# Optimization experiments

Measured on AMD Instinct MI355X. Metric: run time of the kernel, lower is better.

The kernel has to match this reference:

```python
import jax, jax.numpy as jnp
import numpy as np

H = 32        # num_attention_heads (query heads)
G = 8         # num_query_groups (KV heads)
D = 128       # head_dim
HID = 4096    # hidden_size
THETA = 10000.0


def _rope(x, pos):
    # x: [B, h, S, D]; pos: [S]. Rotate-half (LLaMA) convention.
    half = D // 2
    inv_freq = 1.0 / (THETA ** (jnp.arange(0, half, dtype=jnp.float32) / half))
    ang = pos[:, None].astype(jnp.float32) * inv_freq[None, :]   # [S, half]
    cos = jnp.cos(ang)[None, None]                               # [1,1,S,half]
    sin = jnp.sin(ang)[None, None]
    x1, x2 = x[..., :half], x[..., half:]
    return jnp.concatenate([x1 * cos - x2 * sin, x1 * sin + x2 * cos], axis=-1)


def setup_inputs() -> dict:
    key = jax.random.key(0)
    ks = jax.random.split(key, 9)
    s = 0.02
    return {
        "hidden_states": jax.random.normal(ks[0], (1, 2048, HID), jnp.float32),
        "Wq": jax.random.normal(ks[1], (HID, H * D), jnp.float32) * s,
        "bq": jnp.zeros((H * D,), jnp.float32),
        "Wk": jax.random.normal(ks[2], (HID, G * D), jnp.float32) * s,
        "bk": jnp.zeros((G * D,), jnp.float32),
        "Wv": jax.random.normal(ks[3], (HID, G * D), jnp.float32) * s,
        "bv": jnp.zeros((G * D,), jnp.float32),
        "Wo": jax.random.normal(ks[4], (H * D, HID), jnp.float32) * s,
        "bo": jnp.zeros((HID,), jnp.float32),
    }


def reference(hidden_states, Wq, bq, Wk, bk, Wv, bv, Wo, bo):
    B, S, _ = hidden_states.shape
    R = H // G  # query heads per KV group

    q = hidden_states @ Wq + bq  # [B,S,H*D]
    k = hidden_states @ Wk + bk  # [B,S,G*D]
    v = hidden_states @ Wv + bv  # [B,S,G*D]

    q = q.reshape(B, S, H, D).transpose(0, 2, 1, 3)  # [B,H,S,D]
    k = k.reshape(B, S, G, D).transpose(0, 2, 1, 3)  # [B,G,S,D]
    v = v.reshape(B, S, G, D).transpose(0, 2, 1, 3)  # [B,G,S,D]

    pos = jnp.arange(S)
    q = _rope(q, pos)
    k = _rope(k, pos)

    # Grouped attention: broadcast KV across the R query heads of each group
    qg = q.reshape(B, G, R, S, D)
    scores = jnp.einsum('bgrsd,bgtd->bgrst', qg, k) / jnp.sqrt(jnp.float32(D))
    causal = jnp.tril(jnp.ones((S, S), dtype=bool))
    scores = jnp.where(causal[None, None, None], scores, jnp.finfo(scores.dtype).min)
    probs = jax.nn.softmax(scores, axis=-1)
    ctx = jnp.einsum('bgrst,bgtd->bgrsd', probs, v)          # [B,G,R,S,D]
    ctx = ctx.reshape(B, H, S, D).transpose(0, 2, 1, 3).reshape(B, S, H * D)
    return ctx @ Wo + bo
```

## Files before the change

### kernel.cpp

```cpp
#include <hip/hip_runtime.h>
#include <hip/hip_bf16.h>
#include <math.h>

#define HID   4096
#define NH    32
#define NG    8
#define DH    128
#define SEQ   2048
#define QKV_N 6144
#define KOFF  4096
#define VOFF  5120

typedef __bf16 bf16x8 __attribute__((ext_vector_type(8)));
typedef float  f32x4  __attribute__((ext_vector_type(4)));
using bf16 = __hip_bfloat16;

#define LOG2E 1.4426950408889634f
#define SCALE 0.08838834764831845f

typedef const __attribute__((address_space(1))) void* gas_p;
typedef __attribute__((address_space(3))) void* las_p;
__device__ __forceinline__ void async_copy16(void* lds, const void* g) {
  __builtin_amdgcn_global_load_lds((gas_p)g, (las_p)lds, 16, 0, 0);
}

__device__ __forceinline__ unsigned pack2(float a, float b) {
  union { bf16 h[2]; unsigned u; } t;
  t.h[0] = __float2bfloat16(a);
  t.h[1] = __float2bfloat16(b);
  return t.u;
}

__global__ void cast_x_kernel(const float* __restrict__ x, bf16* __restrict__ y, int n4) {
  int i = blockIdx.x * blockDim.x + threadIdx.x;
  if (i >= n4) return;
  float4 v = ((const float4*)x)[i];
  union { bf16 h[4]; uint2 u; } t;
  t.h[0] = __float2bfloat16(v.x);
  t.h[1] = __float2bfloat16(v.y);
  t.h[2] = __float2bfloat16(v.z);
  t.h[3] = __float2bfloat16(v.w);
  ((uint2*)y)[i] = t.u;
}

__global__ __launch_bounds__(256) void wtrans_all_kernel(const float* __restrict__ Wq, const float* __restrict__ Wk,
                                                         const float* __restrict__ Wv, const float* __restrict__ Wo,
                                                         bf16* __restrict__ Wqkv_t, bf16* __restrict__ Wot) {
  __shared__ bf16 T[64][72];
  const int bx = blockIdx.x;
  const float* W; bf16* dst; int N, ntile;
  if (bx < 64)      { W = Wq; dst = Wqkv_t;                      N = 4096; ntile = bx; }
  else if (bx < 80) { W = Wk; dst = Wqkv_t + (size_t)KOFF * HID; N = 1024; ntile = bx - 64; }
  else if (bx < 96) { W = Wv; dst = Wqkv_t + (size_t)VOFF * HID; N = 1024; ntile = bx - 80; }
  else              { W = Wo; dst = Wot;                         N = 4096; ntile = bx - 96; }
  const int n0 = ntile * 64, k0 = blockIdx.y * 64;
  const int t = threadIdx.x;
  const int nn = (t & 15) * 4, kk = t >> 4;
#pragma unroll
  for (int p = 0; p < 4; ++p) {
    const int k = kk + p * 16;
    float4 v = *(const float4*)&W[(size_t)(k0 + k) * N + n0 + nn];
    union { bf16 h[4]; uint2 u; } c;
    c.h[0] = __float2bfloat16(v.x);
    c.h[1] = __float2bfloat16(v.y);
    c.h[2] = __float2bfloat16(v.z);
    c.h[3] = __float2bfloat16(v.w);
    *(uint2*)&T[k][nn] = c.u;
  }
  __syncthreads();
  const int kc = t & 7, nr = t >> 3;
#pragma unroll
  for (int p = 0; p < 2; ++p) {
    const int n = nr + p * 32;
    union { bf16 h[8]; uint4 u; } o;
#pragma unroll
    for (int i = 0; i < 8; ++i) o.h[i] = T[kc * 8 + i][n];
    *(uint4*)&dst[(size_t)(n0 + n) * HID + k0 + kc * 8] = o.u;
  }
}

__global__ void bias_concat_kernel(const float* __restrict__ bq, const float* __restrict__ bk,
                                   const float* __restrict__ bv, float* __restrict__ dst) {
  int i = blockIdx.x * blockDim.x + threadIdx.x;
  if (i < 4096)       dst[i] = bq[i];
  else if (i < 5120)  dst[i] = bk[i - 4096];
  else if (i < 6144)  dst[i] = bv[i - 5120];
}

__device__ __forceinline__ void st_out(float* C, size_t idx, float v) { C[idx] = v; }
__device__ __forceinline__ void st_out(bf16*  C, size_t idx, float v) { C[idx] = __float2bfloat16(v); }

template <typename OutT>
__global__ __launch_bounds__(256) void gemm_bt_kernel(const bf16* __restrict__ A, const bf16* __restrict__ Bt,
                                                      const float* __restrict__ bias, OutT* __restrict__ C,
                                                      int M, int N, int K) {
  __shared__ alignas(16) bf16 As[128][32];
  __shared__ alignas(16) bf16 Bs[128][32];
  const int tid = threadIdx.x;
  const int w = tid >> 6, lane = tid & 63, quad = lane >> 4, l16 = lane & 15;
  const int wr = w >> 1, wc = w & 1;
  const int m0 = blockIdx.y * 128, n0 = blockIdx.x * 128;
  const int srow = lane >> 2;
  const int scol = (lane & 3) * 8;

  f32x4 acc[4][4];
  f32x4 zero4 = {0.f, 0.f, 0.f, 0.f};
#pragma unroll
  for (int mt = 0; mt < 4; ++mt)
#pragma unroll
    for (int nt = 0; nt < 4; ++nt) acc[mt][nt] = zero4;

  const int nIter = K >> 5;
  for (int kb = 0; kb < nIter; ++kb) {
    const int k0 = kb << 5;
#pragma unroll
    for (int c = 0; c < 2; ++c) {
      const int rb = w * 16 + c * 64;
      async_copy16(&As[rb][0], A  + (size_t)(m0 + rb + srow) * K + k0 + scol);
      async_copy16(&Bs[rb][0], Bt + (size_t)(n0 + rb + srow) * K + k0 + scol);
    }
    __syncthreads();
    bf16x8 af[4], bfr[4];
#pragma unroll
    for (int i = 0; i < 4; ++i) {
      af[i]  = *(const bf16x8*)&As[wr * 64 + i * 16 + l16][quad * 8];
      bfr[i] = *(const bf16x8*)&Bs[wc * 64 + i * 16 + l16][quad * 8];
    }
#pragma unroll
    for (int mt = 0; mt < 4; ++mt)
#pragma unroll
      for (int nt = 0; nt < 4; ++nt)
        acc[mt][nt] = __builtin_amdgcn_mfma_f32_16x16x32_bf16(af[mt], bfr[nt], acc[mt][nt], 0, 0, 0);
    __syncthreads();
  }

#pragma unroll
  for (int nt = 0; nt < 4; ++nt) {
    const int col = n0 + wc * 64 + nt * 16 + l16;
    const float bv = bias[col];
#pragma unroll
    for (int mt = 0; mt < 4; ++mt) {
#pragma unroll
      for (int r = 0; r < 4; ++r) {
        const int row = m0 + wr * 64 + mt * 16 + quad * 4 + r;
        st_out(C, (size_t)row * N + col, acc[mt][nt][r] + bv);
      }
    }
  }
}

__global__ __launch_bounds__(256) void rope_vtrans_kernel(bf16* __restrict__ qkv, bf16* __restrict__ vt) {
  __shared__ bf16 tle[32][33];
  const int bx = blockIdx.x;
  const int tid = threadIdx.x;
  if (bx < 2560) {
    int t = bx * 256 + tid;
    int c  = t & 7;
    int hs = (t >> 3) % 40;
    int s  = t / 320;
    int base = (hs < 32) ? hs * 128 : KOFF + (hs - 32) * 128;
    bf16* p = qkv + (size_t)s * QKV_N + base + c * 8;
    union { bf16x8 v; bf16 h[8]; } a, b, ra, rb;
    a.v = *(bf16x8*)p;
    b.v = *(bf16x8*)(p + 64);
#pragma unroll
    for (int j = 0; j < 8; ++j) {
      int d = c * 8 + j;
      float inv = expf(d * -0.14391156862f);
      float ang = (float)s * inv;
      float sn, cs;
      sincosf(ang, &sn, &cs);
      float x1 = __bfloat162float(a.h[j]);
      float x2 = __bfloat162float(b.h[j]);
      ra.h[j] = __float2bfloat16(x1 * cs - x2 * sn);
      rb.h[j] = __float2bfloat16(x1 * sn + x2 * cs);
    }
    *(bf16x8*)p        = ra.v;
    *(bf16x8*)(p + 64) = rb.v;
  } else {
    const int b = bx - 2560;
    const int s0 = (b & 63) * 32, d0 = ((b >> 6) & 3) * 32, g = b >> 8;
    const int tx = tid & 31, ty = tid >> 5;
#pragma unroll
    for (int i = 0; i < 4; ++i)
      tle[ty + i * 8][tx] = qkv[(size_t)(s0 + ty + i * 8) * QKV_N + VOFF + g * 128 + d0 + tx];
    __syncthreads();
#pragma unroll
    for (int i = 0; i < 4; ++i)
      vt[(size_t)(g * 128 + d0 + ty + i * 8) * SEQ + s0 + tx] = tle[tx][ty + i * 8];
  }
}

__global__ __launch_bounds__(256, 2) void attn_kernel(const bf16* __restrict__ qkv, const bf16* __restrict__ vt,
                                                      bf16* __restrict__ ctx) {
  __shared__ bf16 Ks[2][64][128];
  __shared__ bf16 Vs[2][128][64];

  const int bx = blockIdx.x;
  const int h  = blockIdx.y;
  const int g  = h >> 2;
  const int tid = threadIdx.x, w = tid >> 6, lane = tid & 63;
  const int quad = lane >> 4, l16 = lane & 15;
  const int sw = l16 & 7;

  const float c1 = SCALE * LOG2E;
  const float c2 = 12.0f * LOG2E;

  const int addrA = (((quad & 1) << 5) + l16) * 4;
  const int addrB = addrA + 64;
  const bool hiq = quad >= 2;

  f32x4 zero4 = {0.f, 0.f, 0.f, 0.f};

  auto stage = [&](int kt2, int buf) {
    const bf16* kg = qkv + (size_t)(kt2 * 64) * QKV_N + KOFF + g * 128;
    const bf16* vg = vt + (size_t)(g * 128) * SEQ + kt2 * 64;
#pragma unroll
    for (int i = 0; i < 4; ++i) {
      const int c = (i * 4 + w) * 64 + lane;
      {
        const int key = c >> 4, j = c & 15;
        const int js = (j & 8) | ((j ^ key) & 7);
        async_copy16(&Ks[buf][0][0] + (size_t)(i * 4 + w) * 512,
                     kg + (size_t)key * QKV_N + js * 8);
      }
      {
        const int d = c >> 3, k8 = c & 7;
        const int js = (k8 ^ d) & 7;
        async_copy16(&Vs[buf][0][0] + (size_t)(i * 4 + w) * 512,
                     vg + (size_t)d * SEQ + js * 8);
      }
    }
  };

  for (int ph = 0; ph < 2; ++ph) {
    const int qt = ph ? bx : (31 - bx);
    const int n  = qt + 1;

    bf16x8 qf[4];
    {
      const int qrow = qt * 64 + w * 16 + l16;
      const bf16* qp = qkv + (size_t)qrow * QKV_N + h * 128 + quad * 8;
#pragma unroll
      for (int ks = 0; ks < 4; ++ks) qf[ks] = *(const bf16x8*)(qp + ks * 32);
    }

    f32x4 o[8];
#pragma unroll
    for (int dt = 0; dt < 8; ++dt) o[dt] = zero4;
    float rsum = 0.f;

    __syncthreads();
    stage(0, 0);

    for (int kt = 0; kt < n; ++kt) {
      const int cur = kt & 1;
      __syncthreads();
      if (kt + 1 < n) stage(kt + 1, 1 - cur);

      f32x4 s[4];
#pragma unroll
      for (int nt = 0; nt < 4; ++nt) {
        s[nt] = zero4;
#pragma unroll
        for (int ks = 0; ks < 4; ++ks) {
          const int ch = ks * 4 + quad;
          bf16x8 kf = *(const bf16x8*)&Ks[cur][nt * 16 + l16][((ch & 8) | ((ch ^ l16) & 7)) * 8];
          s[nt] = __builtin_amdgcn_mfma_f32_16x16x32_bf16(kf, qf[ks], s[nt], 0, 0, 0);
        }
      }

#pragma unroll
      for (int nt = 0; nt < 4; ++nt)
#pragma unroll
        for (int r = 0; r < 4; ++r)
          s[nt][r] = exp2f(fmaf(s[nt][r], c1, -c2));

      if (kt == qt) {
        const int q_local = w * 16 + l16;
#pragma unroll
        for (int nt = 0; nt < 4; ++nt)
#pragma unroll
          for (int r = 0; r < 4; ++r)
            if (nt * 16 + quad * 4 + r > q_local) s[nt][r] = 0.f;
      }

#pragma unroll
      for (int nt = 0; nt < 4; ++nt)
        rsum += (s[nt][0] + s[nt][1]) + (s[nt][2] + s[nt][3]);

      unsigned pk[4][2];
#pragma unroll
      for (int nt = 0; nt < 4; ++nt) {
        pk[nt][0] = pack2(s[nt][0], s[nt][1]);
        pk[nt][1] = pack2(s[nt][2], s[nt][3]);
      }

#pragma unroll
      for (int k2 = 0; k2 < 2; ++k2) {
        const int lo = 2 * k2, hi = lo + 1;
        int a0l = __builtin_amdgcn_ds_bpermute(addrA, (int)pk[lo][0]);
        int a1l = __builtin_amdgcn_ds_bpermute(addrA, (int)pk[lo][1]);
        int b0l = __builtin_amdgcn_ds_bpermute(addrB, (int)pk[lo][0]);
        int b1l = __builtin_amdgcn_ds_bpermute(addrB, (int)pk[lo][1]);
        int a0h = __builtin_amdgcn_ds_bpermute(addrA, (int)pk[hi][0]);
        int a1h = __builtin_amdgcn_ds_bpermute(addrA, (int)pk[hi][1]);
        int b0h = __builtin_amdgcn_ds_bpermute(addrB, (int)pk[hi][0]);
        int b1h = __builtin_amdgcn_ds_bpermute(addrB, (int)pk[hi][1]);
        union { int u[4]; bf16x8 v; } pf;
        pf.u[0] = hiq ? a0h : a0l;
        pf.u[1] = hiq ? a1h : a1l;
        pf.u[2] = hiq ? b0h : b0l;
        pf.u[3] = hiq ? b1h : b1l;
#pragma unroll
        for (int dt = 0; dt < 8; ++dt) {
          const int ch = k2 * 4 + quad;
          bf16x8 vf = *(const bf16x8*)&Vs[cur][dt * 16 + l16][((ch ^ sw) & 7) * 8];
          o[dt] = __builtin_amdgcn_mfma_f32_16x16x32_bf16(vf, pf.v, o[dt], 0, 0, 0);
        }
      }
    }

    rsum += __shfl_xor(rsum, 16, 64);
    rsum += __shfl_xor(rsum, 32, 64);
    const float inv = 1.0f / rsum;
    const int srow = qt * 64 + w * 16 + l16;
    bf16* cp = ctx + (size_t)srow * HID + h * 128 + quad * 4;
#pragma unroll
    for (int dt = 0; dt < 8; ++dt) {
      union { bf16 h[4]; uint2 u; } ov;
#pragma unroll
      for (int r = 0; r < 4; ++r) ov.h[r] = __float2bfloat16(o[dt][r] * inv);
      *(uint2*)(cp + dt * 16) = ov.u;
    }
  }
}

extern "C" void kernel_launch(void* const* d_in, const int* in_sizes, int n_in,
                              void* d_out, int out_size, void* d_ws, size_t ws_size,
                              hipStream_t stream) {
  const float* X  = (const float*)d_in[0];
  const float* Wq = (const float*)d_in[1];
  const float* bq = (const float*)d_in[2];
  const float* Wk = (const float*)d_in[3];
  const float* bk = (const float*)d_in[4];
  const float* Wv = (const float*)d_in[5];
  const float* bv = (const float*)d_in[6];
  const float* Wo = (const float*)d_in[7];
  const float* bo = (const float*)d_in[8];
  float* out = (float*)d_out;

  char* ws = (char*)d_ws;
  size_t off = 0;
  auto alloc = [&](size_t bytes) { char* p = ws + off; off += (bytes + 255) & ~255ULL; return p; };
  bf16*  Xb     = (bf16*) alloc((size_t)SEQ * HID * 2);
  bf16*  Wqkv_t = (bf16*) alloc((size_t)QKV_N * HID * 2);
  bf16*  Wot    = (bf16*) alloc((size_t)HID * HID * 2);
  float* bqkv   = (float*)alloc((size_t)QKV_N * 4);
  bf16*  QKV    = (bf16*) alloc((size_t)SEQ * QKV_N * 2);
  bf16*  Vt     = (bf16*) alloc((size_t)NG * DH * SEQ * 2);
  bf16*  Ctx    = (bf16*) alloc((size_t)SEQ * HID * 2);

  cast_x_kernel<<<SEQ * HID / 4 / 256, 256, 0, stream>>>(X, Xb, SEQ * HID / 4);
  wtrans_all_kernel<<<dim3(160, HID / 64), 256, 0, stream>>>(Wq, Wk, Wv, Wo, Wqkv_t, Wot);
  bias_concat_kernel<<<QKV_N / 256, 256, 0, stream>>>(bq, bk, bv, bqkv);

  gemm_bt_kernel<bf16><<<dim3(QKV_N / 128, SEQ / 128), 256, 0, stream>>>(Xb, Wqkv_t, bqkv, QKV, SEQ, QKV_N, HID);
  rope_vtrans_kernel<<<2560 + 2048, 256, 0, stream>>>(QKV, Vt);
  attn_kernel<<<dim3(16, NH), 256, 0, stream>>>(QKV, Vt, Ctx);
  gemm_bt_kernel<float><<<dim3(HID / 128, SEQ / 128), 256, 0, stream>>>(Ctx, Wot, bo, out, SEQ, HID, HID);
}
```

Before: 547.6 us.

## Split attention KV tiles across two wave groups, merge prepass kernels, hoist GEMM addressing

The attention kernel now runs 512 threads per block. Two groups of four waves each process a 32-key half of every 64-key tile with their own K/V LDS buffers, and their partial outputs and row sums are combined through shared memory at the end. This is meant to raise parallelism and latency hiding in the attention loop, at the cost of extra reduction traffic and barriers. Separately, the X cast, weight transpose and bias concat kernels are fused into one prepass launch to save launch overhead. The GEMM load addresses are precomputed as pointer increments.

```diff
diff --git a/kernel.cpp b/kernel.cpp
--- a/kernel.cpp
+++ b/kernel.cpp
@@ -31,30 +31,43 @@
   return t.u;
 }
 
-__global__ void cast_x_kernel(const float* __restrict__ x, bf16* __restrict__ y, int n4) {
-  int i = blockIdx.x * blockDim.x + threadIdx.x;
-  if (i >= n4) return;
-  float4 v = ((const float4*)x)[i];
-  union { bf16 h[4]; uint2 u; } t;
-  t.h[0] = __float2bfloat16(v.x);
-  t.h[1] = __float2bfloat16(v.y);
-  t.h[2] = __float2bfloat16(v.z);
-  t.h[3] = __float2bfloat16(v.w);
-  ((uint2*)y)[i] = t.u;
-}
-
-__global__ __launch_bounds__(256) void wtrans_all_kernel(const float* __restrict__ Wq, const float* __restrict__ Wk,
-                                                         const float* __restrict__ Wv, const float* __restrict__ Wo,
-                                                         bf16* __restrict__ Wqkv_t, bf16* __restrict__ Wot) {
+__global__ __launch_bounds__(256) void prepass_kernel(const float* __restrict__ X,
+                                                      const float* __restrict__ Wq, const float* __restrict__ Wk,
+                                                      const float* __restrict__ Wv, const float* __restrict__ Wo,
+                                                      const float* __restrict__ bq, const float* __restrict__ bk,
+                                                      const float* __restrict__ bv,
+                                                      bf16* __restrict__ Xb,
+                                                      bf16* __restrict__ Wqkv_t, bf16* __restrict__ Wot,
+                                                      float* __restrict__ bqkv) {
+  const int bx = blockIdx.x, by = blockIdx.y;
+  const int t = threadIdx.x;
+  if (bx >= 288) {
+    if (by < 24) {
+      int i = by * 256 + t;
+      if (i < 4096)       bqkv[i] = bq[i];
+      else if (i < 5120)  bqkv[i] = bk[i - 4096];
+      else                bqkv[i] = bv[i - 5120];
+    }
+    return;
+  }
+  if (bx >= 160) {
+    int i = ((bx - 160) + 128 * by) * 256 + t;
+    float4 v = ((const float4*)X)[i];
+    union { bf16 h[4]; uint2 u; } c;
+    c.h[0] = __float2bfloat16(v.x);
+    c.h[1] = __float2bfloat16(v.y);
+    c.h[2] = __float2bfloat16(v.z);
+    c.h[3] = __float2bfloat16(v.w);
+    ((uint2*)Xb)[i] = c.u;
+    return;
+  }
   __shared__ bf16 T[64][72];
-  const int bx = blockIdx.x;
   const float* W; bf16* dst; int N, ntile;
   if (bx < 64)      { W = Wq; dst = Wqkv_t;                      N = 4096; ntile = bx; }
   else if (bx < 80) { W = Wk; dst = Wqkv_t + (size_t)KOFF * HID; N = 1024; ntile = bx - 64; }
   else if (bx < 96) { W = Wv; dst = Wqkv_t + (size_t)VOFF * HID; N = 1024; ntile = bx - 80; }
   else              { W = Wo; dst = Wot;                         N = 4096; ntile = bx - 96; }
-  const int n0 = ntile * 64, k0 = blockIdx.y * 64;
-  const int t = threadIdx.x;
+  const int n0 = ntile * 64, k0 = by * 64;
   const int nn = (t & 15) * 4, kk = t >> 4;
 #pragma unroll
   for (int p = 0; p < 4; ++p) {
@@ -77,14 +90,6 @@
     for (int i = 0; i < 8; ++i) o.h[i] = T[kc * 8 + i][n];
     *(uint4*)&dst[(size_t)(n0 + n) * HID + k0 + kc * 8] = o.u;
   }
-}
-
-__global__ void bias_concat_kernel(const float* __restrict__ bq, const float* __restrict__ bk,
-                                   const float* __restrict__ bv, float* __restrict__ dst) {
-  int i = blockIdx.x * blockDim.x + threadIdx.x;
-  if (i < 4096)       dst[i] = bq[i];
-  else if (i < 5120)  dst[i] = bk[i - 4096];
-  else if (i < 6144)  dst[i] = bv[i - 5120];
 }
 
 __device__ __forceinline__ void st_out(float* C, size_t idx, float v) { C[idx] = v; }
@@ -103,6 +108,16 @@
   const int srow = lane >> 2;
   const int scol = (lane & 3) * 8;
 
+  const size_t step64 = (size_t)64 * K;
+  const bf16* pa0 = A  + (size_t)(m0 + w * 16 + srow) * K + scol;
+  const bf16* pa1 = pa0 + step64;
+  const bf16* pb0 = Bt + (size_t)(n0 + w * 16 + srow) * K + scol;
+  const bf16* pb1 = pb0 + step64;
+  bf16* const la0 = &As[w * 16][0];
+  bf16* const la1 = &As[w * 16 + 64][0];
+  bf16* const lb0 = &Bs[w * 16][0];
+  bf16* const lb1 = &Bs[w * 16 + 64][0];
+
   f32x4 acc[4][4];
   f32x4 zero4 = {0.f, 0.f, 0.f, 0.f};
 #pragma unroll
@@ -112,13 +127,11 @@
 
   const int nIter = K >> 5;
   for (int kb = 0; kb < nIter; ++kb) {
-    const int k0 = kb << 5;
-#pragma unroll
-    for (int c = 0; c < 2; ++c) {
-      const int rb = w * 16 + c * 64;
-      async_copy16(&As[rb][0], A  + (size_t)(m0 + rb + srow) * K + k0 + scol);
-      async_copy16(&Bs[rb][0], Bt + (size_t)(n0 + rb + srow) * K + k0 + scol);
-    }
+    async_copy16(la0, pa0);
+    async_copy16(la1, pa1);
+    async_copy16(lb0, pb0);
+    async_copy16(lb1, pb1);
+    pa0 += 32; pa1 += 32; pb0 += 32; pb1 += 32;
     __syncthreads();
     bf16x8 af[4], bfr[4];
 #pragma unroll
@@ -191,17 +204,20 @@
   }
 }
 
-__global__ __launch_bounds__(256, 2) void attn_kernel(const bf16* __restrict__ qkv, const bf16* __restrict__ vt,
+__global__ __launch_bounds__(512, 4) void attn_kernel(const bf16* __restrict__ qkv, const bf16* __restrict__ vt,
                                                       bf16* __restrict__ ctx) {
-  __shared__ bf16 Ks[2][64][128];
-  __shared__ bf16 Vs[2][128][64];
+  __shared__ alignas(16) bf16 Ks[2][2][32][128];
+  __shared__ alignas(16) bf16 Vs[2][2][64][64];
+  __shared__ float rs1[64];
+  float* const red = (float*)&Ks[0][0][0][0];
 
   const int bx = blockIdx.x;
   const int h  = blockIdx.y;
   const int g  = h >> 2;
-  const int tid = threadIdx.x, w = tid >> 6, lane = tid & 63;
-  const int quad = lane >> 4, l16 = lane & 15;
-  const int sw = l16 & 7;
+  const int tid = threadIdx.x;
+  const int w = tid >> 6;
+  const int gid = w >> 2, wq = w & 3;
+  const int lane = tid & 63, quad = lane >> 4, l16 = lane & 15;
 
   const float c1 = SCALE * LOG2E;
   const float c2 = 12.0f * LOG2E;
@@ -213,34 +229,33 @@
   f32x4 zero4 = {0.f, 0.f, 0.f, 0.f};
 
   auto stage = [&](int kt2, int buf) {
-    const bf16* kg = qkv + (size_t)(kt2 * 64) * QKV_N + KOFF + g * 128;
-    const bf16* vg = vt + (size_t)(g * 128) * SEQ + kt2 * 64;
-#pragma unroll
-    for (int i = 0; i < 4; ++i) {
-      const int c = (i * 4 + w) * 64 + lane;
+    const int ktg = 2 * kt2 + gid;
+    const bf16* kg = qkv + (size_t)(ktg * 32) * QKV_N + KOFF + g * 128;
+    const bf16* vg = vt + (size_t)(g * 128) * SEQ + ktg * 32;
+#pragma unroll
+    for (int i = 0; i < 2; ++i) {
+      const int c = (i * 4 + wq) * 64 + lane;
       {
         const int key = c >> 4, j = c & 15;
         const int js = (j & 8) | ((j ^ key) & 7);
-        async_copy16(&Ks[buf][0][0] + (size_t)(i * 4 + w) * 512,
+        async_copy16(&Ks[gid][buf][0][0] + (size_t)(i * 4 + wq) * 512,
                      kg + (size_t)key * QKV_N + js * 8);
       }
       {
-        const int d = c >> 3, k8 = c & 7;
-        const int js = (k8 ^ d) & 7;
-        async_copy16(&Vs[buf][0][0] + (size_t)(i * 4 + w) * 512,
-                     vg + (size_t)d * SEQ + js * 8);
+        const int row = c >> 3, d = row * 2 + ((c >> 2) & 1), k8s = c & 3;
+        const int vjs = (k8s ^ row) & 3;
+        async_copy16(&Vs[gid][buf][0][0] + (size_t)(i * 4 + wq) * 512,
+                     vg + (size_t)d * SEQ + vjs * 8);
       }
     }
   };
 
   for (int ph = 0; ph < 2; ++ph) {
     const int qt = ph ? bx : (31 - bx);
-    const int n  = qt + 1;
 
     bf16x8 qf[4];
     {
-      const int qrow = qt * 64 + w * 16 + l16;
-      const bf16* qp = qkv + (size_t)qrow * QKV_N + h * 128 + quad * 8;
+      const bf16* qp = qkv + (size_t)(qt * 64 + wq * 16 + l16) * QKV_N + h * 128 + quad * 8;
 #pragma unroll
       for (int ks = 0; ks < 4; ++ks) qf[ks] = *(const bf16x8*)(qp + ks * 32);
     }
@@ -253,85 +268,94 @@
     __syncthreads();
     stage(0, 0);
 
-    for (int kt = 0; kt < n; ++kt) {
-      const int cur = kt & 1;
+    for (int kt2 = 0; kt2 <= qt; ++kt2) {
+      const int cur = kt2 & 1;
       __syncthreads();
-      if (kt + 1 < n) stage(kt + 1, 1 - cur);
-
-      f32x4 s[4];
-#pragma unroll
-      for (int nt = 0; nt < 4; ++nt) {
+      if (kt2 + 1 <= qt) stage(kt2 + 1, 1 - cur);
+
+      f32x4 s[2];
+#pragma unroll
+      for (int nt = 0; nt < 2; ++nt) {
         s[nt] = zero4;
 #pragma unroll
         for (int ks = 0; ks < 4; ++ks) {
           const int ch = ks * 4 + quad;
-          bf16x8 kf = *(const bf16x8*)&Ks[cur][nt * 16 + l16][((ch & 8) | ((ch ^ l16) & 7)) * 8];
+          bf16x8 kf = *(const bf16x8*)&Ks[gid][cur][nt * 16 + l16][((ch & 8) | ((ch ^ l16) & 7)) * 8];
           s[nt] = __builtin_amdgcn_mfma_f32_16x16x32_bf16(kf, qf[ks], s[nt], 0, 0, 0);
         }
       }
 
 #pragma unroll
-      for (int nt = 0; nt < 4; ++nt)
+      for (int nt = 0; nt < 2; ++nt)
 #pragma unroll
         for (int r = 0; r < 4; ++r)
           s[nt][r] = exp2f(fmaf(s[nt][r], c1, -c2));
 
-      if (kt == qt) {
-        const int q_local = w * 16 + l16;
-#pragma unroll
-        for (int nt = 0; nt < 4; ++nt)
+      if (kt2 == qt) {
+        const int koff = gid * 32;
+        const int q_local = wq * 16 + l16;
+#pragma unroll
+        for (int nt = 0; nt < 2; ++nt)
 #pragma unroll
           for (int r = 0; r < 4; ++r)
-            if (nt * 16 + quad * 4 + r > q_local) s[nt][r] = 0.f;
-      }
-
-#pragma unroll
-      for (int nt = 0; nt < 4; ++nt)
-        rsum += (s[nt][0] + s[nt][1]) + (s[nt][2] + s[nt][3]);
-
-      unsigned pk[4][2];
-#pragma unroll
-      for (int nt = 0; nt < 4; ++nt) {
+            if (koff + nt * 16 + quad * 4 + r > q_local) s[nt][r] = 0.f;
+      }
+
+      rsum += (s[0][0] + s[0][1]) + (s[0][2] + s[0][3]) +
+              (s[1][0] + s[1][1]) + (s[1][2] + s[1][3]);
+
+      unsigned pk[2][2];
+#pragma unroll
+      for (int nt = 0; nt < 2; ++nt) {
         pk[nt][0] = pack2(s[nt][0], s[nt][1]);
         pk[nt][1] = pack2(s[nt][2], s[nt][3]);
       }
-
-#pragma unroll
-      for (int k2 = 0; k2 < 2; ++k2) {
-        const int lo = 2 * k2, hi = lo + 1;
-        int a0l = __builtin_amdgcn_ds_bpermute(addrA, (int)pk[lo][0]);
-        int a1l = __builtin_amdgcn_ds_bpermute(addrA, (int)pk[lo][1]);
-        int b0l = __builtin_amdgcn_ds_bpermute(addrB, (int)pk[lo][0]);
-        int b1l = __builtin_amdgcn_ds_bpermute(addrB, (int)pk[lo][1]);
-        int a0h = __builtin_amdgcn_ds_bpermute(addrA, (int)pk[hi][0]);
-        int a1h = __builtin_amdgcn_ds_bpermute(addrA, (int)pk[hi][1]);
-        int b0h = __builtin_amdgcn_ds_bpermute(addrB, (int)pk[hi][0]);
-        int b1h = __builtin_amdgcn_ds_bpermute(addrB, (int)pk[hi][1]);
-        union { int u[4]; bf16x8 v; } pf;
-        pf.u[0] = hiq ? a0h : a0l;
-        pf.u[1] = hiq ? a1h : a1l;
-        pf.u[2] = hiq ? b0h : b0l;
-        pf.u[3] = hiq ? b1h : b1l;
-#pragma unroll
-        for (int dt = 0; dt < 8; ++dt) {
-          const int ch = k2 * 4 + quad;
-          bf16x8 vf = *(const bf16x8*)&Vs[cur][dt * 16 + l16][((ch ^ sw) & 7) * 8];
-          o[dt] = __builtin_amdgcn_mfma_f32_16x16x32_bf16(vf, pf.v, o[dt], 0, 0, 0);
-        }
+      int a0l = __builtin_amdgcn_ds_bpermute(addrA, (int)pk[0][0]);
+      int a1l = __builtin_amdgcn_ds_bpermute(addrA, (int)pk[0][1]);
+      int b0l = __builtin_amdgcn_ds_bpermute(addrB, (int)pk[0][0]);
+      int b1l = __builtin_amdgcn_ds_bpermute(addrB, (int)pk[0][1]);
+      int a0h = __builtin_amdgcn_ds_bpermute(addrA, (int)pk[1][0]);
+      int a1h = __builtin_amdgcn_ds_bpermute(addrA, (int)pk[1][1]);
+      int b0h = __builtin_amdgcn_ds_bpermute(addrB, (int)pk[1][0]);
+      int b1h = __builtin_amdgcn_ds_bpermute(addrB, (int)pk[1][1]);
+      union { int u[4]; bf16x8 v; } pf;
+      pf.u[0] = hiq ? a0h : a0l;
+      pf.u[1] = hiq ? a1h : a1l;
+      pf.u[2] = hiq ? b0h : b0l;
+      pf.u[3] = hiq ? b1h : b1l;
+
+#pragma unroll
+      for (int dt = 0; dt < 8; ++dt) {
+        const int d = dt * 16 + l16, row = d >> 1;
+        const int slot = (quad ^ row) & 3;
+        bf16x8 vf = *(const bf16x8*)&Vs[gid][cur][row][(d & 1) * 32 + slot * 8];
+        o[dt] = __builtin_amdgcn_mfma_f32_16x16x32_bf16(vf, pf.v, o[dt], 0, 0, 0);
       }
     }
 
     rsum += __shfl_xor(rsum, 16, 64);
     rsum += __shfl_xor(rsum, 32, 64);
-    const float inv = 1.0f / rsum;
-    const int srow = qt * 64 + w * 16 + l16;
-    bf16* cp = ctx + (size_t)srow * HID + h * 128 + quad * 4;
-#pragma unroll
-    for (int dt = 0; dt < 8; ++dt) {
-      union { bf16 h[4]; uint2 u; } ov;
-#pragma unroll
-      for (int r = 0; r < 4; ++r) ov.h[r] = __float2bfloat16(o[dt][r] * inv);
-      *(uint2*)(cp + dt * 16) = ov.u;
+
+    __syncthreads();
+    if (gid == 1) {
+#pragma unroll
+      for (int dt = 0; dt < 8; ++dt)
+        *(f32x4*)&red[(((wq * 8 + dt) * 64) + lane) * 4] = o[dt];
+      if (quad == 0) rs1[wq * 16 + l16] = rsum;
+    }
+    __syncthreads();
+    if (gid == 0) {
+      const float inv = 1.0f / (rsum + rs1[wq * 16 + l16]);
+      const int srow = qt * 64 + wq * 16 + l16;
+      bf16* cp = ctx + (size_t)srow * HID + h * 128 + quad * 4;
+#pragma unroll
+      for (int dt = 0; dt < 8; ++dt) {
+        f32x4 sum = o[dt] + *(const f32x4*)&red[(((wq * 8 + dt) * 64) + lane) * 4];
+        union { bf16 hh[4]; uint2 u; } ov;
+#pragma unroll
+        for (int r = 0; r < 4; ++r) ov.hh[r] = __float2bfloat16(sum[r] * inv);
+        *(uint2*)(cp + dt * 16) = ov.u;
+      }
     }
   }
 }
@@ -361,12 +385,10 @@
   bf16*  Vt     = (bf16*) alloc((size_t)NG * DH * SEQ * 2);
   bf16*  Ctx    = (bf16*) alloc((size_t)SEQ * HID * 2);
 
-  cast_x_kernel<<<SEQ * HID / 4 / 256, 256, 0, stream>>>(X, Xb, SEQ * HID / 4);
-  wtrans_all_kernel<<<dim3(160, HID / 64), 256, 0, stream>>>(Wq, Wk, Wv, Wo, Wqkv_t, Wot);
-  bias_concat_kernel<<<QKV_N / 256, 256, 0, stream>>>(bq, bk, bv, bqkv);
-
+  prepass_kernel<<<dim3(289, 64), 256, 0, stream>>>(X, Wq, Wk, Wv, Wo, bq, bk, bv,
+                                                    Xb, Wqkv_t, Wot, bqkv);
   gemm_bt_kernel<bf16><<<dim3(QKV_N / 128, SEQ / 128), 256, 0, stream>>>(Xb, Wqkv_t, bqkv, QKV, SEQ, QKV_N, HID);
   rope_vtrans_kernel<<<2560 + 2048, 256, 0, stream>>>(QKV, Vt);
-  attn_kernel<<<dim3(16, NH), 256, 0, stream>>>(QKV, Vt, Ctx);
+  attn_kernel<<<dim3(16, NH), 512, 0, stream>>>(QKV, Vt, Ctx);
   gemm_bt_kernel<float><<<dim3(HID / 128, SEQ / 128), 256, 0, stream>>>(Ctx, Wot, bo, out, SEQ, HID, HID);
 }
```

Measured after the change: 538.5 us. About the same (-1.7%).
